# Kernel optimization log

Hardware: AMD Instinct MI355X
Metric: run time of the kernel (lower is better)

Reference implementation:

```python
import jax, jax.numpy as jnp
import numpy as np

N_HEADS = 4
IN_FEATURES = 1024


def setup_inputs() -> dict:
    key = jax.random.key(0)
    ks = jax.random.split(key, 20)
    B, HW, C = 2, 16384, 1024
    inp = {
        "q": jax.random.normal(ks[0], (B, HW, C), dtype=jnp.float32),
        "k": jax.random.normal(ks[1], (B, HW, C), dtype=jnp.float32),
        "v": jax.random.normal(ks[2], (B, HW, C), dtype=jnp.float32),
    }
    names = ["wqg", "bqg", "wkg", "bkg", "wvg", "bvg",
             "wql", "bql", "wkl", "bkl", "wvl", "bvl", "wp", "bp"]
    for i, n in enumerate(names):
        inp[n] = jax.random.normal(ks[3 + i], (C,), dtype=jnp.float32)
    return inp


def _channel_attention(qm, km, vm, scale):
    # qm/km/vm: (b, hw, c). Attention over the CHANNEL dim per head.
    b, n, c = qm.shape
    d = c // N_HEADS
    qh = qm.reshape(b, n, N_HEADS, d).transpose(0, 2, 3, 1)  # (b, H, d, hw)
    kh = km.reshape(b, n, N_HEADS, d).transpose(0, 2, 3, 1)
    vh = vm.reshape(b, n, N_HEADS, d).transpose(0, 2, 3, 1)
    scores = jnp.einsum("bhdn,bhen->bhde", qh, kh) * scale  # (b, H, d, d)
    attn = jax.nn.softmax(scores, axis=-1)
    out = jnp.einsum("bhde,bhen->bhdn", attn, vh)            # (b, H, d, hw)
    return out.transpose(0, 3, 1, 2).reshape(b, n, c)        # (b, hw, c)


def reference(q, k, v, wqg, bqg, wkg, bkg, wvg, bvg,
              wql, bql, wkl, bkl, wvl, bvl, wp, bp):
    scale = IN_FEATURES ** (-0.5)
    # Depthwise (groups==channels, kernel=1) projections: per-channel affine.
    att_global = _channel_attention(q * wqg + bqg, k * wkg + bkg, v * wvg + bvg, scale)
    # window_size=1 -> local patch extraction is identity; local branch uses its own maps.
    att_local = _channel_attention(q * wql + bql, k * wkl + bkl, v * wvl + bvl, scale)
    att = att_global + att_local
    # Both accumulators hold the same att, so projection input is 2*att.
    return (2.0 * att) * wp + bp
```

## Files before the change

kernel.cpp:

```cpp
#include <hip/hip_runtime.h>
#include <stdint.h>

#define NTOK 16384
#define CDIM 1024
#define DHEAD 256

typedef short s16x8 __attribute__((ext_vector_type(8)));
typedef unsigned short u16x8 __attribute__((ext_vector_type(8)));
typedef _Float16 h16x8 __attribute__((ext_vector_type(8)));
typedef float f32x4 __attribute__((ext_vector_type(4)));

static __device__ __forceinline__ unsigned short f2bf(float f) {
    union { float f; unsigned u; } x; x.f = f;
    unsigned r = (x.u + 0x7fffu + ((x.u >> 16) & 1u)) >> 16;
    return (unsigned short)r;
}
static __device__ __forceinline__ unsigned short f2h(float f) {
    _Float16 h = (_Float16)f;
    return __builtin_bit_cast(unsigned short, h);
}
static __device__ __forceinline__ void lgkm_barrier() {
    asm volatile("s_waitcnt lgkmcnt(0)" ::: "memory");
    __builtin_amdgcn_s_barrier();
}

__global__ __launch_bounds__(512, 2)
void k_gram(const float* __restrict__ q, const float* __restrict__ k,
            unsigned short* __restrict__ Gpart, float* __restrict__ Spart, int nchunk)
{
    __shared__ __align__(16) unsigned short ls[2 * DHEAD * 32];
    unsigned short* lq = ls;
    unsigned short* lk = ls + DHEAD * 32;

    const int t     = threadIdx.x;
    const int bh    = blockIdx.x & 7;
    const int chunk = blockIdx.x >> 3;
    const int b     = bh >> 2, h = bh & 3;
    const int rows  = NTOK / nchunk;
    const int S     = rows >> 5;
    const int n0c   = chunk * rows;

    const int lane = t & 63, w = t >> 6;
    const int isK  = t >> 8;
    const int tl   = t & 255;
    const int ng   = tl & 3;
    const int ch0  = (tl >> 2) * 4;
    const int de0  = (w >> 1) * 64;
    const int e0   = (w & 1) * 128;

    const float* src    = isK ? k : q;
    unsigned short* dst = isK ? lk : lq;
    const float* row0 = src + ((size_t)b * NTOK + n0c + ng * 8) * CDIM + (size_t)h * DHEAD + ch0;

    f32x4 vA[4], vB[4];
#define GL_A(sidx) do { const size_t o_ = (size_t)(sidx) * 32 * CDIM;                \
        _Pragma("unroll") for (int j_ = 0; j_ < 4; ++j_)                              \
            vA[j_] = *reinterpret_cast<const f32x4*>(row0 + o_ + (size_t)j_ * CDIM);   \
        asm volatile("" ::: "memory"); } while (0)
#define GL_B(sidx) do { const size_t o_ = (size_t)(sidx) * 32 * CDIM + 4 * CDIM;     \
        _Pragma("unroll") for (int j_ = 0; j_ < 4; ++j_)                              \
            vB[j_] = *reinterpret_cast<const f32x4*>(row0 + o_ + (size_t)j_ * CDIM);   \
        asm volatile("" ::: "memory"); } while (0)

    GL_A(0);
    GL_B(0);

    float ssum[4] = {0.f, 0.f, 0.f, 0.f};
    f32x4 acc[4][8];
#pragma unroll
    for (int r = 0; r < 4; ++r)
#pragma unroll
        for (int c = 0; c < 8; ++c) acc[r][c] = (f32x4){0.f, 0.f, 0.f, 0.f};

    for (int s = 0; s < S; ++s) {
#pragma unroll
        for (int c = 0; c < 4; ++c) {
            const int ch = ch0 + c;
            ushort4 p;
            p.x = f2bf(vA[0][c]); p.y = f2bf(vA[1][c]);
            p.z = f2bf(vA[2][c]); p.w = f2bf(vA[3][c]);
            ssum[c] += (vA[0][c] + vA[1][c]) + (vA[2][c] + vA[3][c]);
            *reinterpret_cast<ushort4*>(&dst[ch * 32 + ((ng ^ ((ch >> 1) & 3)) * 8)]) = p;
        }
        if (s + 1 < S) GL_A(s + 1);

#pragma unroll
        for (int c = 0; c < 4; ++c) {
            const int ch = ch0 + c;
            ushort4 p;
            p.x = f2bf(vB[0][c]); p.y = f2bf(vB[1][c]);
            p.z = f2bf(vB[2][c]); p.w = f2bf(vB[3][c]);
            ssum[c] += (vB[0][c] + vB[1][c]) + (vB[2][c] + vB[3][c]);
            *reinterpret_cast<ushort4*>(&dst[ch * 32 + ((ng ^ ((ch >> 1) & 3)) * 8) + 4]) = p;
        }
        if (s + 1 < S) GL_B(s + 1);

        lgkm_barrier();

        {
            s16x8 af[4], bfr[8];
            const int slot = lane >> 4;
#pragma unroll
            for (int r = 0; r < 4; ++r) {
                const int row = de0 + r * 16 + (lane & 15);
                af[r] = *reinterpret_cast<const s16x8*>(&lq[row * 32 + ((slot ^ ((row >> 1) & 3)) * 8)]);
            }
#pragma unroll
            for (int c = 0; c < 8; ++c) {
                const int row = e0 + c * 16 + (lane & 15);
                bfr[c] = *reinterpret_cast<const s16x8*>(&lk[row * 32 + ((slot ^ ((row >> 1) & 3)) * 8)]);
            }
#pragma unroll
            for (int r = 0; r < 4; ++r)
#pragma unroll
                for (int c = 0; c < 8; ++c)
                    acc[r][c] = __builtin_amdgcn_mfma_f32_16x16x32_bf16(af[r], bfr[c], acc[r][c], 0, 0, 0);
        }
        lgkm_barrier();
    }
#undef GL_A
#undef GL_B

#pragma unroll
    for (int off = 1; off < 4; off <<= 1)
#pragma unroll
        for (int c = 0; c < 4; ++c) ssum[c] += __shfl_xor(ssum[c], off);
    if ((lane & 3) == 0) {
        float* sp = Spart + (size_t)(bh * nchunk + chunk) * 512 + isK * 256;
        *reinterpret_cast<float4*>(&sp[ch0]) = make_float4(ssum[0], ssum[1], ssum[2], ssum[3]);
    }

    unsigned short* gp = Gpart + (size_t)(bh * nchunk + chunk) * 65536;
#pragma unroll
    for (int qtr = 0; qtr < 4; ++qtr) {
        if ((w >> 1) == qtr) {
#pragma unroll
            for (int r = 0; r < 4; ++r) {
                const int de_l = r * 16 + (lane >> 4) * 4;
#pragma unroll
                for (int c = 0; c < 8; ++c) {
                    const int e = e0 + c * 16 + (lane & 15);
#pragma unroll
                    for (int reg = 0; reg < 4; ++reg)
                        ls[(de_l + reg) * 256 + e] = f2h(acc[r][c][reg]);
                }
            }
        }
        lgkm_barrier();
#pragma unroll
        for (int i = 0; i < 4; ++i) {
            const int idx = i * 512 + t;
            *reinterpret_cast<u16x8*>(gp + qtr * 16384 + idx * 8) =
                *reinterpret_cast<const u16x8*>(&ls[idx * 8]);
        }
        lgkm_barrier();
    }
}

__global__ __launch_bounds__(256)
void k_scores(const unsigned short* __restrict__ Gpart, const float* __restrict__ Spart,
              const float* __restrict__ wqg, const float* __restrict__ bqg,
              const float* __restrict__ wkg, const float* __restrict__ bkg,
              const float* __restrict__ wvg, const float* __restrict__ bvg,
              const float* __restrict__ wql, const float* __restrict__ bql,
              const float* __restrict__ wkl, const float* __restrict__ bkl,
              const float* __restrict__ wvl, const float* __restrict__ bvl,
              const float* __restrict__ wp,  const float* __restrict__ bp,
              unsigned short* __restrict__ Wm, float* __restrict__ beta, int nchunk)
{
    __shared__ float sSq[256], sSk[256];
    const int t  = threadIdx.x;
    const int bh = blockIdx.x >> 5;
    const int rg = blockIdx.x & 31;
    const int h  = bh & 3;

    float aq = 0.f, ak = 0.f;
    for (int c = 0; c < nchunk; ++c) {
        const float* sp = Spart + (size_t)(bh * nchunk + c) * 512;
        aq += sp[t]; ak += sp[256 + t];
    }
    sSq[t] = aq; sSk[t] = ak;
    __syncthreads();

    const int dl  = t >> 5;
    const int de  = rg * 8 + dl;
    const int e8  = (t & 31) * 8;
    const int cd  = h * DHEAD + de;
    const int ce0 = h * DHEAD + e8;

    float g[8] = {0.f, 0.f, 0.f, 0.f, 0.f, 0.f, 0.f, 0.f};
    const unsigned short* gpb = Gpart + (size_t)bh * nchunk * 65536 + (size_t)de * 256 + e8;
    for (int c = 0; c < nchunk; ++c) {
        h16x8 v = *reinterpret_cast<const h16x8*>(gpb + (size_t)c * 65536);
#pragma unroll
        for (int j = 0; j < 8; ++j) g[j] += (float)v[j];
    }

    const float sqv = sSq[de];
    float skv[8];
#pragma unroll
    for (int j = 0; j < 8; ++j) skv[j] = sSk[e8 + j];

    float wrow[8] = {0.f, 0.f, 0.f, 0.f, 0.f, 0.f, 0.f, 0.f};
    float bacc = 0.f;
    const float scale = 0.03125f;
#pragma unroll
    for (int br = 0; br < 2; ++br) {
        const float* wq = br ? wql : wqg;  const float* bq = br ? bql : bqg;
        const float* wk = br ? wkl : wkg;  const float* bk = br ? bkl : bkg;
        const float* wv = br ? wvl : wvg;  const float* bv = br ? bvl : bvg;
        const float wqv = wq[cd], bqv = bq[cd];

        float s[8], m = -1e30f;
#pragma unroll
        for (int j = 0; j < 8; ++j) {
            const float wkv = wk[ce0 + j], bkv = bk[ce0 + j];
            s[j] = scale * (wqv * wkv * g[j] + wqv * bkv * sqv
                            + bqv * wkv * skv[j] + bqv * bkv * 16384.0f);
            m = fmaxf(m, s[j]);
        }
#pragma unroll
        for (int off = 16; off; off >>= 1) m = fmaxf(m, __shfl_xor(m, off));
        float p[8], sum = 0.f;
#pragma unroll
        for (int j = 0; j < 8; ++j) { p[j] = __expf(s[j] - m); sum += p[j]; }
#pragma unroll
        for (int off = 16; off; off >>= 1) sum += __shfl_xor(sum, off);
        const float inv = 1.f / sum;
#pragma unroll
        for (int j = 0; j < 8; ++j) {
            const float a = p[j] * inv;
            wrow[j] += a * wv[ce0 + j];
            bacc    += a * bv[ce0 + j];
        }
    }
    const float wp2 = 2.f * wp[cd];
    u16x8 pw;
#pragma unroll
    for (int j = 0; j < 8; ++j) pw[j] = f2bf(wp2 * wrow[j]);
    *reinterpret_cast<u16x8*>(Wm + (size_t)bh * 65536 + (size_t)de * 256 + e8) = pw;
#pragma unroll
    for (int off = 16; off; off >>= 1) bacc += __shfl_xor(bacc, off);
    if ((t & 31) == 0) beta[bh * 256 + de] = wp2 * bacc + bp[cd];
}

__global__ __launch_bounds__(256, 3)
void k_out(const float* __restrict__ v, const unsigned short* __restrict__ Wm,
           const float* __restrict__ beta, float* __restrict__ out)
{
    __shared__ __align__(16) unsigned short lv[64 * 256];
    const int t    = threadIdx.x;
    const int bh   = blockIdx.x & 7;
    const int tile = blockIdx.x >> 3;
    const int b    = bh >> 2, h = bh & 3;
    const int n0   = tile * 64;

#pragma unroll
    for (int i = 0; i < 8; ++i) {
        const int sf = i * 256 + t;
        const int n  = sf >> 5, s = sf & 31;
        const float* vp = v + ((size_t)b * NTOK + n0 + n) * CDIM + (size_t)h * DHEAD + s * 8;
        const float4 v0 = *reinterpret_cast<const float4*>(vp);
        const float4 v1 = *reinterpret_cast<const float4*>(vp + 4);
        const int idx = n * 256 + ((s ^ (n & 7)) * 8);
        *reinterpret_cast<ushort4*>(&lv[idx])     = make_ushort4(f2bf(v0.x), f2bf(v0.y), f2bf(v0.z), f2bf(v0.w));
        *reinterpret_cast<ushort4*>(&lv[idx + 4]) = make_ushort4(f2bf(v1.x), f2bf(v1.y), f2bf(v1.z), f2bf(v1.w));
    }
    __syncthreads();

    const int w = t >> 6, lane = t & 63;
    const int nw  = (w >> 1) * 32;
    const int dd0 = (w & 1) * 128;
    const unsigned short* Wg = Wm + (size_t)bh * 65536;

    f32x4 acc[2][8];
#pragma unroll
    for (int r = 0; r < 2; ++r)
#pragma unroll
        for (int c = 0; c < 8; ++c) acc[r][c] = (f32x4){0.f, 0.f, 0.f, 0.f};

#pragma unroll
    for (int ks = 0; ks < 8; ++ks) {
        const int e0 = ks * 32;
        s16x8 af[2], bfr[8];
#pragma unroll
        for (int r = 0; r < 2; ++r) {
            const int n  = nw + r * 16 + (lane & 15);
            const int sg = (e0 >> 3) + (lane >> 4);
            af[r] = *reinterpret_cast<const s16x8*>(&lv[n * 256 + ((sg ^ (n & 7)) * 8)]);
        }
#pragma unroll
        for (int c = 0; c < 8; ++c) {
            const int dd = dd0 + c * 16 + (lane & 15);
            const int e  = e0 + (lane >> 4) * 8;
            bfr[c] = *reinterpret_cast<const s16x8*>(Wg + (size_t)dd * 256 + e);
        }
#pragma unroll
        for (int r = 0; r < 2; ++r)
#pragma unroll
            for (int c = 0; c < 8; ++c)
                acc[r][c] = __builtin_amdgcn_mfma_f32_16x16x32_bf16(af[r], bfr[c], acc[r][c], 0, 0, 0);
    }

    float betar[8];
#pragma unroll
    for (int c = 0; c < 8; ++c) betar[c] = beta[bh * 256 + dd0 + c * 16 + (lane & 15)];

#pragma unroll
    for (int r = 0; r < 2; ++r)
#pragma unroll
        for (int c = 0; c < 8; ++c) {
            const int dd = dd0 + c * 16 + (lane & 15);
#pragma unroll
            for (int reg = 0; reg < 4; ++reg) {
                const int n = nw + r * 16 + (lane >> 4) * 4 + reg;
                out[((size_t)b * NTOK + n0 + n) * CDIM + (size_t)h * DHEAD + dd] =
                    acc[r][c][reg] + betar[c];
            }
        }
}

extern "C" void kernel_launch(void* const* d_in, const int* in_sizes, int n_in,
                              void* d_out, int out_size, void* d_ws, size_t ws_size,
                              hipStream_t stream)
{
    const float* q = (const float*)d_in[0];
    const float* k = (const float*)d_in[1];
    const float* v = (const float*)d_in[2];
    const float* wgt[14];
    for (int i = 0; i < 14; ++i) wgt[i] = (const float*)d_in[3 + i];
    float* out = (float*)d_out;

    int nchunk = 32;
    while (nchunk > 1) {
        size_t need = (size_t)8 * nchunk * 65536 * 2
                    + (size_t)8 * nchunk * 512 * 4
                    + (size_t)8 * 65536 * 2
                    + (size_t)8 * 256 * 4 + 1024;
        if (need <= ws_size) break;
        nchunk >>= 1;
    }

    char* p = (char*)d_ws;
    unsigned short* Gpart = (unsigned short*)p; p += (size_t)8 * nchunk * 65536 * 2;
    float* Spart = (float*)p;                   p += (size_t)8 * nchunk * 512 * 4;
    unsigned short* Wm = (unsigned short*)p;    p += (size_t)8 * 65536 * 2;
    float* beta  = (float*)p;

    k_gram<<<dim3(8 * nchunk), dim3(512), 0, stream>>>(q, k, Gpart, Spart, nchunk);
    k_scores<<<dim3(8 * 32), dim3(256), 0, stream>>>(
        Gpart, Spart,
        wgt[0], wgt[1], wgt[2], wgt[3], wgt[4], wgt[5],
        wgt[6], wgt[7], wgt[8], wgt[9], wgt[10], wgt[11],
        wgt[12], wgt[13], Wm, beta, nchunk);
    k_out<<<dim3(8 * 256), dim3(256), 0, stream>>>(v, Wm, beta, out);
}
```

Baseline: 185.7 us.

## Stream q/k tiles straight to LDS with double-buffered async loads in k_gram

k_gram now uses global_load_lds to copy fp32 q/k tiles straight into a double-buffered 128KB dynamic LDS region, with a manual vmcnt wait so the next tile loads while the current one is computed. The fp32-to-bf16 conversion and the per-channel sums move to the LDS-read side, and a swizzled read layout replaces the old register staging. This aims to cut register pressure and the serialized convert-then-store step, overlapping HBM traffic with MFMA work. It needs a large dynamic LDS allocation, which limits k_gram to one block per CU. k_out's launch bounds are also raised to 4 blocks per CU.

```diff
diff --git a/kernel.cpp b/kernel.cpp
--- a/kernel.cpp
+++ b/kernel.cpp
@@ -28,9 +28,9 @@
 void k_gram(const float* __restrict__ q, const float* __restrict__ k,
             unsigned short* __restrict__ Gpart, float* __restrict__ Spart, int nchunk)
 {
-    __shared__ __align__(16) unsigned short ls[2 * DHEAD * 32];
-    unsigned short* lq = ls;
-    unsigned short* lk = ls + DHEAD * 32;
+    extern __shared__ __align__(16) float lds[];
+    float* lq = lds;
+    float* lk = lds + 2 * 32 * 256;
 
     const int t     = threadIdx.x;
     const int bh    = blockIdx.x & 7;
@@ -41,31 +41,49 @@
     const int n0c   = chunk * rows;
 
     const int lane = t & 63, w = t >> 6;
-    const int isK  = t >> 8;
-    const int tl   = t & 255;
-    const int ng   = tl & 3;
-    const int ch0  = (tl >> 2) * 4;
-    const int de0  = (w >> 1) * 64;
-    const int e0   = (w & 1) * 128;
-
-    const float* src    = isK ? k : q;
-    unsigned short* dst = isK ? lk : lq;
-    const float* row0 = src + ((size_t)b * NTOK + n0c + ng * 8) * CDIM + (size_t)h * DHEAD + ch0;
-
-    f32x4 vA[4], vB[4];
-#define GL_A(sidx) do { const size_t o_ = (size_t)(sidx) * 32 * CDIM;                \
-        _Pragma("unroll") for (int j_ = 0; j_ < 4; ++j_)                              \
-            vA[j_] = *reinterpret_cast<const f32x4*>(row0 + o_ + (size_t)j_ * CDIM);   \
-        asm volatile("" ::: "memory"); } while (0)
-#define GL_B(sidx) do { const size_t o_ = (size_t)(sidx) * 32 * CDIM + 4 * CDIM;     \
-        _Pragma("unroll") for (int j_ = 0; j_ < 4; ++j_)                              \
-            vB[j_] = *reinterpret_cast<const f32x4*>(row0 + o_ + (size_t)j_ * CDIM);   \
-        asm volatile("" ::: "memory"); } while (0)
-
-    GL_A(0);
-    GL_B(0);
-
-    float ssum[4] = {0.f, 0.f, 0.f, 0.f};
+    const int g = lane >> 4, li = lane & 15;
+    const int de0 = (w >> 1) * 64;
+    const int e0  = (w & 1) * 128;
+
+    const float* qbase = q + ((size_t)b * NTOK + n0c) * CDIM + h * DHEAD;
+    const float* kbase = k + ((size_t)b * NTOK + n0c) * CDIM + h * DHEAD;
+
+    const int src_off0 = lane << 2;
+    const int src_off1 = (lane ^ 4) << 2;
+
+#define STAGE(sidx, buf) do {                                                        \
+        _Pragma("unroll") for (int i_ = 0; i_ < 4; ++i_) {                            \
+            const int row_ = w * 4 + i_;                                              \
+            const int so_  = ((row_ >> 3) & 1) ? src_off1 : src_off0;                 \
+            const size_t go_ = (size_t)((sidx) * 32 + row_) * CDIM + so_;             \
+            __builtin_amdgcn_global_load_lds(                                         \
+                (const __attribute__((address_space(1))) unsigned int*)(qbase + go_), \
+                (__attribute__((address_space(3))) unsigned int*)(lq + (buf) * 8192 + row_ * 256), \
+                16, 0, 0);                                                            \
+            __builtin_amdgcn_global_load_lds(                                         \
+                (const __attribute__((address_space(1))) unsigned int*)(kbase + go_), \
+                (__attribute__((address_space(3))) unsigned int*)(lk + (buf) * 8192 + row_ * 256), \
+                16, 0, 0);                                                            \
+        } } while (0)
+
+    const int swzg = (g & 1) << 2;
+    int aoff[4], boff[8];
+#pragma unroll
+    for (int r = 0; r < 4; ++r) {
+        const int ch = de0 + r * 16 + li;
+        aoff[r] = ((((ch >> 2) ^ swzg) << 2) | (ch & 3));
+    }
+#pragma unroll
+    for (int c = 0; c < 8; ++c) {
+        const int e = e0 + c * 16 + li;
+        boff[c] = ((((e >> 2) ^ swzg) << 2) | (e & 3));
+    }
+    const int rowf = g * 8 * 256;
+
+    STAGE(0, 0);
+
+    float sq[4] = {0.f, 0.f, 0.f, 0.f};
+    float sk[8] = {0.f, 0.f, 0.f, 0.f, 0.f, 0.f, 0.f, 0.f};
     f32x4 acc[4][8];
 #pragma unroll
     for (int r = 0; r < 4; ++r)
@@ -73,73 +91,82 @@
         for (int c = 0; c < 8; ++c) acc[r][c] = (f32x4){0.f, 0.f, 0.f, 0.f};
 
     for (int s = 0; s < S; ++s) {
-#pragma unroll
-        for (int c = 0; c < 4; ++c) {
-            const int ch = ch0 + c;
-            ushort4 p;
-            p.x = f2bf(vA[0][c]); p.y = f2bf(vA[1][c]);
-            p.z = f2bf(vA[2][c]); p.w = f2bf(vA[3][c]);
-            ssum[c] += (vA[0][c] + vA[1][c]) + (vA[2][c] + vA[3][c]);
-            *reinterpret_cast<ushort4*>(&dst[ch * 32 + ((ng ^ ((ch >> 1) & 3)) * 8)]) = p;
-        }
-        if (s + 1 < S) GL_A(s + 1);
-
-#pragma unroll
-        for (int c = 0; c < 4; ++c) {
-            const int ch = ch0 + c;
-            ushort4 p;
-            p.x = f2bf(vB[0][c]); p.y = f2bf(vB[1][c]);
-            p.z = f2bf(vB[2][c]); p.w = f2bf(vB[3][c]);
-            ssum[c] += (vB[0][c] + vB[1][c]) + (vB[2][c] + vB[3][c]);
-            *reinterpret_cast<ushort4*>(&dst[ch * 32 + ((ng ^ ((ch >> 1) & 3)) * 8) + 4]) = p;
-        }
-        if (s + 1 < S) GL_B(s + 1);
+        const int cur = s & 1;
+        if (s + 1 < S) {
+            STAGE(s + 1, cur ^ 1);
+            asm volatile("s_waitcnt vmcnt(8)" ::: "memory");
+        } else {
+            asm volatile("s_waitcnt vmcnt(0)" ::: "memory");
+        }
+        __builtin_amdgcn_s_barrier();
+
+        const float* bq = lq + cur * 8192 + rowf;
+        const float* bk = lk + cur * 8192 + rowf;
+        s16x8 af[4], bfr[8];
+#pragma unroll
+        for (int r = 0; r < 4; ++r) {
+            u16x8 p;
+            float ssum = 0.f;
+#pragma unroll
+            for (int j = 0; j < 8; ++j) {
+                const float x = bq[j * 256 + aoff[r]];
+                ssum += x;
+                p[j] = f2bf(x);
+            }
+            if ((w & 1) == 0) sq[r] += ssum;
+            af[r] = __builtin_bit_cast(s16x8, p);
+        }
+#pragma unroll
+        for (int c = 0; c < 8; ++c) {
+            u16x8 p;
+            float ssum = 0.f;
+#pragma unroll
+            for (int j = 0; j < 8; ++j) {
+                const float x = bk[j * 256 + boff[c]];
+                ssum += x;
+                p[j] = f2bf(x);
+            }
+            if (w < 2) sk[c] += ssum;
+            bfr[c] = __builtin_bit_cast(s16x8, p);
+        }
+#pragma unroll
+        for (int r = 0; r < 4; ++r)
+#pragma unroll
+            for (int c = 0; c < 8; ++c)
+                acc[r][c] = __builtin_amdgcn_mfma_f32_16x16x32_bf16(af[r], bfr[c], acc[r][c], 0, 0, 0);
 
         lgkm_barrier();
-
-        {
-            s16x8 af[4], bfr[8];
-            const int slot = lane >> 4;
-#pragma unroll
-            for (int r = 0; r < 4; ++r) {
-                const int row = de0 + r * 16 + (lane & 15);
-                af[r] = *reinterpret_cast<const s16x8*>(&lq[row * 32 + ((slot ^ ((row >> 1) & 3)) * 8)]);
-            }
-#pragma unroll
-            for (int c = 0; c < 8; ++c) {
-                const int row = e0 + c * 16 + (lane & 15);
-                bfr[c] = *reinterpret_cast<const s16x8*>(&lk[row * 32 + ((slot ^ ((row >> 1) & 3)) * 8)]);
-            }
-#pragma unroll
-            for (int r = 0; r < 4; ++r)
-#pragma unroll
-                for (int c = 0; c < 8; ++c)
-                    acc[r][c] = __builtin_amdgcn_mfma_f32_16x16x32_bf16(af[r], bfr[c], acc[r][c], 0, 0, 0);
-        }
-        lgkm_barrier();
-    }
-#undef GL_A
-#undef GL_B
-
-#pragma unroll
-    for (int off = 1; off < 4; off <<= 1)
-#pragma unroll
-        for (int c = 0; c < 4; ++c) ssum[c] += __shfl_xor(ssum[c], off);
-    if ((lane & 3) == 0) {
-        float* sp = Spart + (size_t)(bh * nchunk + chunk) * 512 + isK * 256;
-        *reinterpret_cast<float4*>(&sp[ch0]) = make_float4(ssum[0], ssum[1], ssum[2], ssum[3]);
-    }
-
+    }
+#undef STAGE
+
+#pragma unroll
+    for (int off = 16; off < 64; off <<= 1) {
+#pragma unroll
+        for (int r = 0; r < 4; ++r) sq[r] += __shfl_xor(sq[r], off);
+#pragma unroll
+        for (int c = 0; c < 8; ++c) sk[c] += __shfl_xor(sk[c], off);
+    }
+    float* sp = Spart + (size_t)(bh * nchunk + chunk) * 512;
+    if (((w & 1) == 0) && g == 0) {
+#pragma unroll
+        for (int r = 0; r < 4; ++r) sp[de0 + r * 16 + li] = sq[r];
+    }
+    if (w < 2 && g == 0) {
+#pragma unroll
+        for (int c = 0; c < 8; ++c) sp[256 + e0 + c * 16 + li] = sk[c];
+    }
+
+    unsigned short* ls = (unsigned short*)lds;
     unsigned short* gp = Gpart + (size_t)(bh * nchunk + chunk) * 65536;
 #pragma unroll
     for (int qtr = 0; qtr < 4; ++qtr) {
         if ((w >> 1) == qtr) {
 #pragma unroll
             for (int r = 0; r < 4; ++r) {
-                const int de_l = r * 16 + (lane >> 4) * 4;
+                const int de_l = r * 16 + g * 4;
 #pragma unroll
                 for (int c = 0; c < 8; ++c) {
-                    const int e = e0 + c * 16 + (lane & 15);
+                    const int e = e0 + c * 16 + li;
 #pragma unroll
                     for (int reg = 0; reg < 4; ++reg)
                         ls[(de_l + reg) * 256 + e] = f2h(acc[r][c][reg]);
@@ -244,7 +271,7 @@
     if ((t & 31) == 0) beta[bh * 256 + de] = wp2 * bacc + bp[cd];
 }
 
-__global__ __launch_bounds__(256, 3)
+__global__ __launch_bounds__(256, 4)
 void k_out(const float* __restrict__ v, const unsigned short* __restrict__ Wm,
            const float* __restrict__ beta, float* __restrict__ out)
 {
@@ -347,7 +374,7 @@
     unsigned short* Wm = (unsigned short*)p;    p += (size_t)8 * 65536 * 2;
     float* beta  = (float*)p;
 
-    k_gram<<<dim3(8 * nchunk), dim3(512), 0, stream>>>(q, k, Gpart, Spart, nchunk);
+    k_gram<<<dim3(8 * nchunk), dim3(512), 131072, stream>>>(q, k, Gpart, Spart, nchunk);
     k_scores<<<dim3(8 * 32), dim3(256), 0, stream>>>(
         Gpart, Spart,
         wgt[0], wgt[1], wgt[2], wgt[3], wgt[4], wgt[5],
```

After: 212.5 us. 14.4% more time.

## Rewrite output GEMM with register-direct 32x32 MFMA and double-buffered loads

Applied to the files above, without the earlier changes.

The output kernel no longer stages v through shared memory. Each wave loads fp32 v directly into registers, converts it with packed bf16 conversion instructions, and feeds 32x32x16 MFMAs, while the next k-step's A and B fragments are prefetched in software. The tile grows to 128 tokens per block with half the grid, removing the LDS round trip and barrier in exchange for more registers (occupancy bound lowered to 2) and B fragments read uncached from global or L2 per wave. The output store pattern also changes: each lane now writes a column across 16 rows.

```diff
diff --git a/kernel.cpp b/kernel.cpp
--- a/kernel.cpp
+++ b/kernel.cpp
@@ -9,6 +9,7 @@
 typedef unsigned short u16x8 __attribute__((ext_vector_type(8)));
 typedef _Float16 h16x8 __attribute__((ext_vector_type(8)));
 typedef float f32x4 __attribute__((ext_vector_type(4)));
+typedef float f32x16 __attribute__((ext_vector_type(16)));
 
 static __device__ __forceinline__ unsigned short f2bf(float f) {
     union { float f; unsigned u; } x; x.f = f;
@@ -18,6 +19,11 @@
 static __device__ __forceinline__ unsigned short f2h(float f) {
     _Float16 h = (_Float16)f;
     return __builtin_bit_cast(unsigned short, h);
+}
+static __device__ __forceinline__ unsigned cvtpk(float lo, float hi) {
+    unsigned r;
+    asm("v_cvt_pk_bf16_f32 %0, %1, %2" : "=v"(r) : "v"(lo), "v"(hi));
+    return r;
 }
 static __device__ __forceinline__ void lgkm_barrier() {
     asm volatile("s_waitcnt lgkmcnt(0)" ::: "memory");
@@ -166,7 +172,7 @@
               const float* __restrict__ wkl, const float* __restrict__ bkl,
               const float* __restrict__ wvl, const float* __restrict__ bvl,
               const float* __restrict__ wp,  const float* __restrict__ bp,
-              unsigned short* __restrict__ Wm, float* __restrict__ beta, int nchunk)
+              unsigned short* __restrict__ Wf, float* __restrict__ beta, int nchunk)
 {
     __shared__ float sSq[256], sSk[256];
     const int t  = threadIdx.x;
@@ -211,19 +217,19 @@
         const float* wv = br ? wvl : wvg;  const float* bv = br ? bvl : bvg;
         const float wqv = wq[cd], bqv = bq[cd];
 
-        float s[8], m = -1e30f;
+        float s[8], mm = -1e30f;
 #pragma unroll
         for (int j = 0; j < 8; ++j) {
             const float wkv = wk[ce0 + j], bkv = bk[ce0 + j];
             s[j] = scale * (wqv * wkv * g[j] + wqv * bkv * sqv
                             + bqv * wkv * skv[j] + bqv * bkv * 16384.0f);
-            m = fmaxf(m, s[j]);
-        }
-#pragma unroll
-        for (int off = 16; off; off >>= 1) m = fmaxf(m, __shfl_xor(m, off));
+            mm = fmaxf(mm, s[j]);
+        }
+#pragma unroll
+        for (int off = 16; off; off >>= 1) mm = fmaxf(mm, __shfl_xor(mm, off));
         float p[8], sum = 0.f;
 #pragma unroll
-        for (int j = 0; j < 8; ++j) { p[j] = __expf(s[j] - m); sum += p[j]; }
+        for (int j = 0; j < 8; ++j) { p[j] = __expf(s[j] - mm); sum += p[j]; }
 #pragma unroll
         for (int off = 16; off; off >>= 1) sum += __shfl_xor(sum, off);
         const float inv = 1.f / sum;
@@ -238,86 +244,76 @@
     u16x8 pw;
 #pragma unroll
     for (int j = 0; j < 8; ++j) pw[j] = f2bf(wp2 * wrow[j]);
-    *reinterpret_cast<u16x8*>(Wm + (size_t)bh * 65536 + (size_t)de * 256 + e8) = pw;
+    *reinterpret_cast<u16x8*>(Wf + (size_t)bh * 65536 + (size_t)de * 256 + e8) = pw;
 #pragma unroll
     for (int off = 16; off; off >>= 1) bacc += __shfl_xor(bacc, off);
     if ((t & 31) == 0) beta[bh * 256 + de] = wp2 * bacc + bp[cd];
 }
 
-__global__ __launch_bounds__(256, 3)
-void k_out(const float* __restrict__ v, const unsigned short* __restrict__ Wm,
+__global__ __launch_bounds__(256, 2)
+void k_out(const float* __restrict__ v, const unsigned short* __restrict__ Wf,
            const float* __restrict__ beta, float* __restrict__ out)
 {
-    __shared__ __align__(16) unsigned short lv[64 * 256];
-    const int t    = threadIdx.x;
-    const int bh   = blockIdx.x & 7;
-    const int tile = blockIdx.x >> 3;
+    const int P    = blockIdx.x;
+    const int bh   = P & 7;
+    const int tile = P >> 3;
     const int b    = bh >> 2, h = bh & 3;
-    const int n0   = tile * 64;
-
-#pragma unroll
-    for (int i = 0; i < 8; ++i) {
-        const int sf = i * 256 + t;
-        const int n  = sf >> 5, s = sf & 31;
-        const float* vp = v + ((size_t)b * NTOK + n0 + n) * CDIM + (size_t)h * DHEAD + s * 8;
-        const float4 v0 = *reinterpret_cast<const float4*>(vp);
-        const float4 v1 = *reinterpret_cast<const float4*>(vp + 4);
-        const int idx = n * 256 + ((s ^ (n & 7)) * 8);
-        *reinterpret_cast<ushort4*>(&lv[idx])     = make_ushort4(f2bf(v0.x), f2bf(v0.y), f2bf(v0.z), f2bf(v0.w));
-        *reinterpret_cast<ushort4*>(&lv[idx + 4]) = make_ushort4(f2bf(v1.x), f2bf(v1.y), f2bf(v1.z), f2bf(v1.w));
-    }
-    __syncthreads();
-
+
+    const int t = threadIdx.x;
     const int w = t >> 6, lane = t & 63;
-    const int nw  = (w >> 1) * 32;
-    const int dd0 = (w & 1) * 128;
-    const unsigned short* Wg = Wm + (size_t)bh * 65536;
-
-    f32x4 acc[2][8];
-#pragma unroll
-    for (int r = 0; r < 2; ++r)
-#pragma unroll
-        for (int c = 0; c < 8; ++c) acc[r][c] = (f32x4){0.f, 0.f, 0.f, 0.f};
-
-#pragma unroll
-    for (int ks = 0; ks < 8; ++ks) {
-        const int e0 = ks * 32;
-        s16x8 af[2], bfr[8];
-#pragma unroll
-        for (int r = 0; r < 2; ++r) {
-            const int n  = nw + r * 16 + (lane & 15);
-            const int sg = (e0 >> 3) + (lane >> 4);
-            af[r] = *reinterpret_cast<const s16x8*>(&lv[n * 256 + ((sg ^ (n & 7)) * 8)]);
-        }
-#pragma unroll
-        for (int c = 0; c < 8; ++c) {
-            const int dd = dd0 + c * 16 + (lane & 15);
-            const int e  = e0 + (lane >> 4) * 8;
-            bfr[c] = *reinterpret_cast<const s16x8*>(Wg + (size_t)dd * 256 + e);
-        }
-#pragma unroll
-        for (int r = 0; r < 2; ++r)
-#pragma unroll
-            for (int c = 0; c < 8; ++c)
-                acc[r][c] = __builtin_amdgcn_mfma_f32_16x16x32_bf16(af[r], bfr[c], acc[r][c], 0, 0, 0);
-    }
-
-    float betar[8];
-#pragma unroll
-    for (int c = 0; c < 8; ++c) betar[c] = beta[bh * 256 + dd0 + c * 16 + (lane & 15)];
-
-#pragma unroll
-    for (int r = 0; r < 2; ++r)
-#pragma unroll
-        for (int c = 0; c < 8; ++c) {
-            const int dd = dd0 + c * 16 + (lane & 15);
-#pragma unroll
-            for (int reg = 0; reg < 4; ++reg) {
-                const int n = nw + r * 16 + (lane >> 4) * 4 + reg;
-                out[((size_t)b * NTOK + n0 + n) * CDIM + (size_t)h * DHEAD + dd] =
-                    acc[r][c][reg] + betar[c];
-            }
-        }
+    const int l31 = lane & 31, g2 = lane >> 5;
+    const int n0 = tile * 128 + w * 32;
+
+    const float* pv = v + (size_t)(b * NTOK + n0 + l31) * CDIM + h * DHEAD + g2 * 8;
+    const unsigned short* pw = Wf + (size_t)bh * 65536 + (size_t)l31 * 256 + g2 * 8;
+
+    f32x4 Aa[2], Ab[2];
+    u16x8 Ba[8], Bb[8];
+
+#define LDSTEP(av, bv2, ks) do {                                              \
+        av[0] = *reinterpret_cast<const f32x4*>(pv + (ks) * 16);               \
+        av[1] = *reinterpret_cast<const f32x4*>(pv + (ks) * 16 + 4);           \
+        _Pragma("unroll") for (int dg = 0; dg < 8; ++dg)                       \
+            bv2[dg] = *reinterpret_cast<const u16x8*>(pw + (size_t)dg * 8192 + (ks) * 16); \
+    } while (0)
+
+    f32x16 acc[8];
+#pragma unroll
+    for (int dg = 0; dg < 8; ++dg)
+#pragma unroll
+        for (int j = 0; j < 16; ++j) acc[dg][j] = 0.f;
+
+#define CPSTEP(av, bv2) do {                                                  \
+        int4 A;                                                               \
+        A.x = cvtpk(av[0][0], av[0][1]); A.y = cvtpk(av[0][2], av[0][3]);     \
+        A.z = cvtpk(av[1][0], av[1][1]); A.w = cvtpk(av[1][2], av[1][3]);     \
+        const s16x8 fA = __builtin_bit_cast(s16x8, A);                        \
+        _Pragma("unroll") for (int dg = 0; dg < 8; ++dg)                      \
+            acc[dg] = __builtin_amdgcn_mfma_f32_32x32x16_bf16(                \
+                fA, __builtin_bit_cast(s16x8, bv2[dg]), acc[dg], 0, 0, 0);    \
+    } while (0)
+
+    LDSTEP(Aa, Ba, 0);
+#pragma unroll
+    for (int ks = 0; ks < 16; ks += 2) {
+        if (ks + 1 < 16) LDSTEP(Ab, Bb, ks + 1);
+        CPSTEP(Aa, Ba);
+        if (ks + 2 < 16) LDSTEP(Aa, Ba, ks + 2);
+        if (ks + 1 < 16) CPSTEP(Ab, Bb);
+    }
+#undef LDSTEP
+#undef CPSTEP
+
+#pragma unroll
+    for (int dg = 0; dg < 8; ++dg) {
+        const float bb = beta[bh * 256 + dg * 32 + l31];
+#pragma unroll
+        for (int reg = 0; reg < 16; ++reg) {
+            const int row = (reg & 3) + 8 * (reg >> 2) + 4 * g2;
+            out[(size_t)(b * NTOK + n0 + row) * CDIM + h * DHEAD + dg * 32 + l31] =
+                acc[dg][reg] + bb;
+        }
+    }
 }
 
 extern "C" void kernel_launch(void* const* d_in, const int* in_sizes, int n_in,
@@ -344,7 +340,7 @@
     char* p = (char*)d_ws;
     unsigned short* Gpart = (unsigned short*)p; p += (size_t)8 * nchunk * 65536 * 2;
     float* Spart = (float*)p;                   p += (size_t)8 * nchunk * 512 * 4;
-    unsigned short* Wm = (unsigned short*)p;    p += (size_t)8 * 65536 * 2;
+    unsigned short* Wf = (unsigned short*)p;    p += (size_t)8 * 65536 * 2;
     float* beta  = (float*)p;
 
     k_gram<<<dim3(8 * nchunk), dim3(512), 0, stream>>>(q, k, Gpart, Spart, nchunk);
@@ -352,6 +348,6 @@
         Gpart, Spart,
         wgt[0], wgt[1], wgt[2], wgt[3], wgt[4], wgt[5],
         wgt[6], wgt[7], wgt[8], wgt[9], wgt[10], wgt[11],
-        wgt[12], wgt[13], Wm, beta, nchunk);
-    k_out<<<dim3(8 * 256), dim3(256), 0, stream>>>(v, Wm, beta, out);
-}
+        wgt[12], wgt[13], Wf, beta, nchunk);
+    k_out<<<dim3(8 * 128), dim3(256), 0, stream>>>(v, Wf, beta, out);
+}
```

After: 193.9 us. 1.04x slower.
